# Kernel tuning notes

Hardware: AMD Instinct MI355X
Metric: run time of the kernel (lower is better)

Reference implementation:

```python
import jax, jax.numpy as jnp
import numpy as np

B, S, D = 8, 1024, 768
H, DK = 12, 64
DFF = 3072
EPS = 1e-5


def setup_inputs() -> dict:
    key = jax.random.key(0)
    ks = jax.random.split(key, 12)
    s = lambda fan_in: 1.0 / np.sqrt(fan_in)
    return {
        "x": jax.random.normal(ks[0], (B, S, D), jnp.float32),
        "Wq": jax.random.normal(ks[1], (D, D), jnp.float32) * s(D),
        "Wk": jax.random.normal(ks[2], (D, D), jnp.float32) * s(D),
        "Wv": jax.random.normal(ks[3], (D, D), jnp.float32) * s(D),
        "Wo": jax.random.normal(ks[4], (D, D), jnp.float32) * s(D),
        "g1": jnp.ones((D,), jnp.float32),
        "b1": jnp.zeros((D,), jnp.float32),
        "g2": jnp.ones((D,), jnp.float32),
        "b2": jnp.zeros((D,), jnp.float32),
        "W1": jax.random.normal(ks[5], (D, DFF), jnp.float32) * s(D),
        "bW1": jnp.zeros((DFF,), jnp.float32),
        "W2": jax.random.normal(ks[6], (DFF, D), jnp.float32) * s(DFF),
        "bW2": jnp.zeros((D,), jnp.float32),
    }


def _layernorm(x, g, b):
    mu = x.mean(-1, keepdims=True)
    var = ((x - mu) ** 2).mean(-1, keepdims=True)
    return (x - mu) * jax.lax.rsqrt(var + EPS) * g + b


def reference(x, Wq, Wk, Wv, Wo, g1, b1, g2, b2, W1, bW1, W2, bW2):
    scale = DK ** (-0.5)
    # pre-norm attention block
    h = _layernorm(x, g1, b1)
    q = (h @ Wq).reshape(B, S, H, DK)
    k = (h @ Wk).reshape(B, S, H, DK)
    v = (h @ Wv).reshape(B, S, H, DK)
    logits = jnp.einsum("bqhd,bkhd->bhqk", q, k) * scale  # [B,H,S,S]
    weights = jax.nn.softmax(logits, axis=-1)
    attn = jnp.einsum("bhqk,bkhd->bqhd", weights, v).reshape(B, S, D)
    x = x + attn @ Wo
    # pre-norm FFN block
    h = _layernorm(x, g2, b2)
    h = jax.nn.gelu(h @ W1 + bW1, approximate=False)
    x = x + h @ W2 + bW2
    return x
```

## Files before the change

kernel.cpp:

```cpp
#include <hip/hip_runtime.h>
#include <cstdint>
#include <cstddef>

#define B_   8
#define S_   1024
#define D_   768
#define H_   12
#define DK_  64
#define DFF_ 3072
#define M_   (B_*S_)

typedef __attribute__((ext_vector_type(8))) short  short8;
typedef __attribute__((ext_vector_type(4))) short  short4v;
typedef __attribute__((ext_vector_type(8))) __bf16 bf16x8;
typedef __attribute__((ext_vector_type(4))) float  f32x4;
typedef __attribute__((ext_vector_type(4))) unsigned uint4v;
typedef __attribute__((ext_vector_type(2))) unsigned uint2v;

__device__ __forceinline__ unsigned short f2bf(float f) {
    unsigned u = __builtin_bit_cast(unsigned, f);
    u += 0x7FFFu + ((u >> 16) & 1u);
    return (unsigned short)(u >> 16);
}

__device__ __forceinline__ unsigned pkbf(float a, float b) {
    unsigned short ua = __builtin_bit_cast(unsigned short, (__bf16)a);
    unsigned short ub = __builtin_bit_cast(unsigned short, (__bf16)b);
    return (unsigned)ua | ((unsigned)ub << 16);
}

__device__ __forceinline__ f32x4 mfma16(short8 a, short8 b, f32x4 c) {
    return __builtin_amdgcn_mfma_f32_16x16x32_bf16(
        __builtin_bit_cast(bf16x8, a), __builtin_bit_cast(bf16x8, b), c, 0, 0, 0);
}

__device__ __forceinline__ void gload16(const void* g, void* l) {
    auto gp = reinterpret_cast<const __attribute__((address_space(1))) unsigned*>(
        reinterpret_cast<uintptr_t>(g));
    auto lp = reinterpret_cast<__attribute__((address_space(3))) unsigned*>(
        reinterpret_cast<uintptr_t>(l));
    __builtin_amdgcn_global_load_lds(gp, lp, 16, 0, 0);
}

__device__ __forceinline__ float gelu_fast(float v) {
    float w = v * __builtin_fmaf(v * v, 0.044715f, 1.0f);
    float e = __builtin_amdgcn_exp2f(-2.3021178f * w);
    return v * __builtin_amdgcn_rcpf(1.0f + e);
}

__global__ __launch_bounds__(256) void wtrans12_kernel(
    const float* __restrict__ Wq, const float* __restrict__ Wk,
    const float* __restrict__ Wv, const float* __restrict__ Wo,
    const float* __restrict__ W1, const float* __restrict__ W2,
    unsigned short* __restrict__ wt_qkv, unsigned short* __restrict__ wt_1,
    unsigned short* __restrict__ wt_2)
{
    __shared__ float tile[32][33];
    const int z = blockIdx.z;
    const float* src; unsigned short* dst; int sstride, dstride;
    if (z < 4) {
        src = (z == 0) ? Wq : (z == 1) ? Wk : (z == 2) ? Wv : Wo;
        dst = wt_qkv + (size_t)z * 768 * 768;
        sstride = 768; dstride = 768;
    } else if (z < 8) {
        int q = z - 4;
        src = W1 + q * 768;
        dst = wt_1 + (size_t)q * 768 * 768;
        sstride = 3072; dstride = 768;
    } else {
        int q = z - 8;
        src = W2 + (size_t)q * 768 * 768;
        dst = wt_2 + q * 768;
        sstride = 768; dstride = 3072;
    }
    const int n0 = blockIdx.x * 32, k0 = blockIdx.y * 32;
    const int tx = threadIdx.x, ty = threadIdx.y;
#pragma unroll
    for (int j = 0; j < 4; ++j)
        tile[ty + j*8][tx] = src[(size_t)(k0 + ty + j*8) * sstride + n0 + tx];
    __syncthreads();
#pragma unroll
    for (int j = 0; j < 4; ++j)
        dst[(size_t)(n0 + ty + j*8) * dstride + k0 + tx] = f2bf(tile[tx][ty + j*8]);
}

__global__ __launch_bounds__(256) void ln_kernel(
    const float* __restrict__ x, const float* __restrict__ g,
    const float* __restrict__ b, unsigned short* __restrict__ out)
{
    int row = blockIdx.x, t = threadIdx.x;
    const float* xr = x + (size_t)row * D_;
    float v[3];
#pragma unroll
    for (int i = 0; i < 3; ++i) v[i] = xr[t + i*256];
    float s  = v[0] + v[1] + v[2];
    float ss = v[0]*v[0] + v[1]*v[1] + v[2]*v[2];
#pragma unroll
    for (int d = 1; d < 64; d <<= 1) { s += __shfl_xor(s, d); ss += __shfl_xor(ss, d); }
    __shared__ float red[8];
    int w = t >> 6, lane = t & 63;
    if (lane == 0) { red[w] = s; red[4 + w] = ss; }
    __syncthreads();
    s  = red[0] + red[1] + red[2] + red[3];
    ss = red[4] + red[5] + red[6] + red[7];
    float mu   = s * (1.0f / D_);
    float var  = ss * (1.0f / D_) - mu * mu;
    float rstd = rsqrtf(var + 1e-5f);
    unsigned short* orow = out + (size_t)row * D_;
#pragma unroll
    for (int i = 0; i < 3; ++i) {
        int c = t + i*256;
        orow[c] = f2bf((v[i] - mu) * rstd * g[c] + b[c]);
    }
}

template<int BN, int EPI>
__global__ __launch_bounds__(256, 2) void gemm_kernel(
    const unsigned short* __restrict__ A, const unsigned short* __restrict__ Wt,
    const float* __restrict__ bias, const float* __restrict__ resid,
    void* __restrict__ outp, int N, int K)
{
    __shared__ unsigned short Al[2][128*64];
    __shared__ unsigned short Bl[2][BN*64];
    constexpr int NJ = BN / 64;
    constexpr int ASH = 4, BSH = 2*NJ;
    const int nwg = gridDim.x;
    const int p = blockIdx.x;
    const int cpx = nwg >> 3;
    const int xcd = p & 7, id = p >> 3;
    const int nbn = N / BN;
    const int rowsX = cpx / nbn;
    const int hn = nbn >> 1, hc = cpx >> 1;
    const int half = id / hc, rr = id % hc;
    const int bm = xcd * rowsX + rr / hn;
    const int bn = half * hn + rr % hn;

    const int t = threadIdx.x;
    const int lane = t & 63, w = t >> 6;
    const int wm = w >> 1, wn = w & 1;
    const int lr = lane & 15, lh = lane >> 4;
    const char* aBase = (const char*)(A  + (size_t)(bm*128) * K);
    const char* bBase = (const char*)(Wt + (size_t)(bn*BN)  * K);

    uintptr_t aAdr[ASH], bAdr[BSH];
#pragma unroll
    for (int s = 0; s < ASH; ++s) {
        int d = s*4096 + t*16;
        int row = d >> 7;
        int ch  = ((d >> 4) & 7) ^ (row & 7);
        aAdr[s] = (uintptr_t)aBase + (size_t)row*(K*2) + ch*16;
    }
#pragma unroll
    for (int s = 0; s < BSH; ++s) {
        int d = s*4096 + t*16;
        int row = d >> 7;
        int ch  = ((d >> 4) & 7) ^ (row & 7);
        bAdr[s] = (uintptr_t)bBase + (size_t)row*(K*2) + ch*16;
    }

    f32x4 acc[4][2*NJ] = {};

    auto stage = [&](int kt, int buf) {
        const int k0b = kt << 7;
#pragma unroll
        for (int s = 0; s < ASH; ++s)
            gload16((const void*)(aAdr[s] + k0b), (char*)&Al[buf][0] + s*4096 + t*16);
#pragma unroll
        for (int s = 0; s < BSH; ++s)
            gload16((const void*)(bAdr[s] + k0b), (char*)&Bl[buf][0] + s*4096 + t*16);
    };

    const int nk = K >> 6;
    stage(0, 0);
    stage(1, 1);

    for (int it = 0; it < nk; ++it) {
        const int buf = it & 1;
        if (it + 1 < nk) {
            if constexpr (BN == 128) asm volatile("s_waitcnt vmcnt(8)" ::: "memory");
            else                     asm volatile("s_waitcnt vmcnt(6)" ::: "memory");
        } else {
            asm volatile("s_waitcnt vmcnt(0)" ::: "memory");
        }
        __builtin_amdgcn_s_barrier();

        short8 xf[2][4], wf[2][2*NJ];
#pragma unroll
        for (int kk = 0; kk < 2; ++kk) {
#pragma unroll
            for (int i = 0; i < 4; ++i)
                xf[kk][i] = *reinterpret_cast<const short8*>(
                    &Al[buf][(wm*64 + i*16 + lr)*64 + (((kk*4 + lh) ^ (lr & 7))*8)]);
#pragma unroll
            for (int j = 0; j < 2*NJ; ++j)
                wf[kk][j] = *reinterpret_cast<const short8*>(
                    &Bl[buf][(wn*(32*NJ) + j*16 + lr)*64 + (((kk*4 + lh) ^ (lr & 7))*8)]);
        }
        __builtin_amdgcn_s_setprio(1);
#pragma unroll
        for (int kk = 0; kk < 2; ++kk)
#pragma unroll
            for (int i = 0; i < 4; ++i)
#pragma unroll
                for (int j = 0; j < 2*NJ; ++j)
                    acc[i][j] = mfma16(wf[kk][j], xf[kk][i], acc[i][j]);
        __builtin_amdgcn_s_setprio(0);
        __builtin_amdgcn_s_barrier();
        if (it + 2 < nk) stage(it + 2, buf);
    }

#pragma unroll
    for (int i = 0; i < 4; ++i) {
        const int m = bm*128 + wm*64 + i*16 + lr;
#pragma unroll
        for (int j = 0; j < 2*NJ; ++j) {
            const int n0 = bn*BN + wn*(32*NJ) + j*16 + lh*4;
            f32x4 v = acc[i][j];
            if (EPI == 1) {
                f32x4 bb = *reinterpret_cast<const f32x4*>(&bias[n0]);
                v += bb;
#pragma unroll
                for (int r = 0; r < 4; ++r) v[r] = gelu_fast(v[r]);
            }
            if (EPI == 2) {
                if (bias) v += *reinterpret_cast<const f32x4*>(&bias[n0]);
                v += *reinterpret_cast<const f32x4*>(&resid[(size_t)m*N + n0]);
                *reinterpret_cast<f32x4*>(&((float*)outp)[(size_t)m*N + n0]) = v;
            } else {
                uint2v pv = { pkbf(v[0], v[1]), pkbf(v[2], v[3]) };
                *reinterpret_cast<uint2v*>(&((unsigned short*)outp)[(size_t)m*N + n0]) = pv;
            }
        }
    }
}

__global__ __launch_bounds__(256) void vtrans_kernel(
    const unsigned short* __restrict__ qkv, unsigned short* __restrict__ vt)
{
    __shared__ unsigned short tl[64][65];
    int bid = blockIdx.x;
    int sblk = bid & 15, bh = bid >> 4;
    int b = bh / H_, h = bh % H_;
    int t = threadIdx.x, tx = t & 63, ty = t >> 6;
    int s0 = sblk * 64;
#pragma unroll
    for (int j = 0; j < 16; ++j) {
        int s = j*4 + ty;
        tl[s][tx] = qkv[(size_t)(b*S_ + s0 + s)*2304 + 1536 + h*64 + tx];
    }
    __syncthreads();
#pragma unroll
    for (int j = 0; j < 16; ++j) {
        int dk = j*4 + ty;
        vt[((size_t)bh*64 + dk)*S_ + s0 + tx] = tl[tx][dk];
    }
}

__global__ __launch_bounds__(512) void attn_kernel(
    const unsigned short* __restrict__ qkv, const unsigned short* __restrict__ vt,
    unsigned short* __restrict__ out)
{
    __shared__ unsigned short Kl[2][64*64];
    __shared__ unsigned short Vl[2][64*64];

    const int p = blockIdx.x;
    const int l = (p & 7) * 48 + (p >> 3);
    const int qb = l & 3, bh = l >> 2;
    const int b = bh / H_, h = bh % H_;
    const int t = threadIdx.x, lane = t & 63, w = t >> 6;
    const int lr = lane & 15, lh = lane >> 4;
    const int sz = (lr & 7) << 3;

    const float SC = 0.125f * 1.44269504089f;
    const float SHIFT = 12.0f;

    const int qrow0 = qb*256 + w*32;
    short8 bq[2][2];
#pragma unroll
    for (int qi = 0; qi < 2; ++qi) {
        const unsigned short* qp = qkv + (size_t)(b*S_ + qrow0 + qi*16 + lr)*2304 + h*64;
#pragma unroll
        for (int c = 0; c < 2; ++c)
            bq[qi][c] = *reinterpret_cast<const short8*>(&qp[c*32 + lh*8]);
    }

    float l_run[2] = {0.f, 0.f};
    f32x4 o[2][4] = {};

    uintptr_t kAdr, vAdr;
    {
        int d = t*16;
        int row = d >> 7;
        int sc = (d & 127) ^ ((row & 7) << 4);
        kAdr = (uintptr_t)qkv + ((size_t)(b*S_ + row)*2304 + 768 + h*64)*2 + sc;
        vAdr = (uintptr_t)vt  + ((size_t)(bh*64 + row)*1024)*2 + sc;
    }

    auto stage = [&](int kb, int buf) {
        const size_t kOff = (size_t)kb * 64 * 2304 * 2;
        const size_t vOff = (size_t)kb * 128;
        gload16((const void*)(kAdr + kOff), (char*)&Kl[buf][0] + t*16);
        gload16((const void*)(vAdr + vOff), (char*)&Vl[buf][0] + t*16);
    };

    stage(0, 0);
    asm volatile("s_waitcnt vmcnt(0)" ::: "memory");
    __builtin_amdgcn_s_barrier();

    for (int kb = 0; kb < 16; ++kb) {
        const int buf = kb & 1;
        if (kb < 15) stage(kb + 1, buf ^ 1);

        short8 ak[4][2];
#pragma unroll
        for (int j = 0; j < 4; ++j)
#pragma unroll
            for (int c = 0; c < 2; ++c)
                ak[j][c] = *reinterpret_cast<const short8*>(
                    &Kl[buf][(j*16 + lr)*64 + ((c*32 + lh*8) ^ sz)]);

        short8 av[4][2];
#pragma unroll
        for (int j = 0; j < 4; ++j) {
            const unsigned short* vrow = &Vl[buf][(j*16 + lr)*64];
#pragma unroll
            for (int ks = 0; ks < 2; ++ks) {
                short4v lo = *reinterpret_cast<const short4v*>(&vrow[(ks*32 + lh*4)      ^ sz]);
                short4v hi = *reinterpret_cast<const short4v*>(&vrow[(ks*32 + 16 + lh*4) ^ sz]);
                av[j][ks] = __builtin_shufflevector(lo, hi, 0,1,2,3,4,5,6,7);
            }
        }

#pragma unroll
        for (int qi = 0; qi < 2; ++qi) {
            f32x4 s[4];
            __builtin_amdgcn_s_setprio(1);
#pragma unroll
            for (int j = 0; j < 4; ++j) {
                f32x4 z = {0.f, 0.f, 0.f, 0.f};
                z = mfma16(ak[j][0], bq[qi][0], z);
                z = mfma16(ak[j][1], bq[qi][1], z);
                s[j] = z;
            }
            __builtin_amdgcn_s_setprio(0);

            float rs = 0.f;
#pragma unroll
            for (int j = 0; j < 4; ++j)
#pragma unroll
                for (int r = 0; r < 4; ++r) {
                    float pv = __builtin_amdgcn_exp2f(
                        __builtin_fmaf(s[j][r], SC, -SHIFT));
                    s[j][r] = pv;
                    rs += pv;
                }
            l_run[qi] += rs;

            uint4v u0 = { pkbf(s[0][0], s[0][1]), pkbf(s[0][2], s[0][3]),
                          pkbf(s[1][0], s[1][1]), pkbf(s[1][2], s[1][3]) };
            uint4v u1 = { pkbf(s[2][0], s[2][1]), pkbf(s[2][2], s[2][3]),
                          pkbf(s[3][0], s[3][1]), pkbf(s[3][2], s[3][3]) };
            short8 pb0 = __builtin_bit_cast(short8, u0);
            short8 pb1 = __builtin_bit_cast(short8, u1);

            __builtin_amdgcn_s_setprio(1);
#pragma unroll
            for (int j = 0; j < 4; ++j) {
                o[qi][j] = mfma16(av[j][0], pb0, o[qi][j]);
                o[qi][j] = mfma16(av[j][1], pb1, o[qi][j]);
            }
            __builtin_amdgcn_s_setprio(0);
        }

        asm volatile("s_waitcnt vmcnt(0)" ::: "memory");
        __builtin_amdgcn_s_barrier();
    }

#pragma unroll
    for (int qi = 0; qi < 2; ++qi) {
        float ls = l_run[qi];
        ls += __shfl_xor(ls, 16);
        ls += __shfl_xor(ls, 32);
        float inv = 1.0f / ls;
        int q = qrow0 + qi*16 + lr;
        unsigned short* orow = out + (size_t)(b*S_ + q)*D_ + h*64;
#pragma unroll
        for (int j = 0; j < 4; ++j) {
            uint2v vv = { pkbf(o[qi][j][0]*inv, o[qi][j][1]*inv),
                          pkbf(o[qi][j][2]*inv, o[qi][j][3]*inv) };
            *reinterpret_cast<uint2v*>(&orow[j*16 + lh*4]) = vv;
        }
    }
}

extern "C" void kernel_launch(void* const* d_in, const int* in_sizes, int n_in,
                              void* d_out, int out_size, void* d_ws, size_t ws_size,
                              hipStream_t stream)
{
    (void)in_sizes; (void)n_in; (void)out_size; (void)ws_size;
    const float* x   = (const float*)d_in[0];
    const float* Wq  = (const float*)d_in[1];
    const float* Wk  = (const float*)d_in[2];
    const float* Wv  = (const float*)d_in[3];
    const float* Wo  = (const float*)d_in[4];
    const float* g1  = (const float*)d_in[5];
    const float* b1  = (const float*)d_in[6];
    const float* g2  = (const float*)d_in[7];
    const float* b2  = (const float*)d_in[8];
    const float* W1  = (const float*)d_in[9];
    const float* bW1 = (const float*)d_in[10];
    const float* W2  = (const float*)d_in[11];
    const float* bW2 = (const float*)d_in[12];
    float* out = (float*)d_out;

    char* ws = (char*)d_ws;
    unsigned short* wt_qkv = (unsigned short*)(ws);
    unsigned short* wt_o   = (unsigned short*)(ws + 3538944);
    unsigned short* wt_1   = (unsigned short*)(ws + 4718592);
    unsigned short* wt_2   = (unsigned short*)(ws + 9437184);
    unsigned short* slotA  = (unsigned short*)(ws + 14155776);
    unsigned short* qkv    = (unsigned short*)(ws + 26738688);
    unsigned short* vt     = (unsigned short*)(ws + 64487424);
    unsigned short* ffm    = qkv;

    dim3 tb(32, 8);
    wtrans12_kernel<<<dim3(24,24,12), tb, 0, stream>>>(
        Wq, Wk, Wv, Wo, W1, W2, wt_qkv, wt_1, wt_2);

    ln_kernel<<<M_, 256, 0, stream>>>(x, g1, b1, slotA);
    gemm_kernel<128,0><<<1152, 256, 0, stream>>>(slotA, wt_qkv, nullptr, nullptr, qkv, 2304, 768);
    vtrans_kernel<<<1536, 256, 0, stream>>>(qkv, vt);
    attn_kernel<<<384, 512, 0, stream>>>(qkv, vt, slotA);
    gemm_kernel<64,2><<<768, 256, 0, stream>>>(slotA, wt_o, nullptr, x, (void*)out, 768, 768);
    ln_kernel<<<M_, 256, 0, stream>>>(out, g2, b2, slotA);
    gemm_kernel<128,1><<<1536, 256, 0, stream>>>(slotA, wt_1, bW1, nullptr, ffm, 3072, 768);
    gemm_kernel<64,2><<<768, 256, 0, stream>>>(ffm, wt_2, bW2, out, (void*)out, 768, 3072);
}
```

Before: 272.3 us.

## Pre-permute V transpose for single 16B LDS reads; halve attention block size

The V-transpose kernel now writes each 64-key chunk in a permuted column order. This lets the attention kernel load each V fragment with one 16-byte LDS read instead of two 8-byte reads plus a shuffle. The attention launch also changes from 384 blocks of 512 threads covering 256 query rows to 768 blocks of 256 threads covering 128 rows, with each thread staging two K/V chunks. The launch bound requests 3 blocks per CU. Smaller blocks should help occupancy and load balance, at the cost of reloading K/V tiles twice as often per query row.

```diff
diff --git a/kernel.cpp b/kernel.cpp
--- a/kernel.cpp
+++ b/kernel.cpp
@@ -11,7 +11,6 @@
 #define M_   (B_*S_)
 
 typedef __attribute__((ext_vector_type(8))) short  short8;
-typedef __attribute__((ext_vector_type(4))) short  short4v;
 typedef __attribute__((ext_vector_type(8))) __bf16 bf16x8;
 typedef __attribute__((ext_vector_type(4))) float  f32x4;
 typedef __attribute__((ext_vector_type(4))) unsigned uint4v;
@@ -249,14 +248,17 @@
         tl[s][tx] = qkv[(size_t)(b*S_ + s0 + s)*2304 + 1536 + h*64 + tx];
     }
     __syncthreads();
+    const int lh2 = (tx >> 3) & 3, e2 = tx & 7;
+    const int psrc = (tx & 32) |
+        ((e2 < 4) ? (lh2*4 + e2) : (16 + lh2*4 + (e2 - 4)));
 #pragma unroll
     for (int j = 0; j < 16; ++j) {
         int dk = j*4 + ty;
-        vt[((size_t)bh*64 + dk)*S_ + s0 + tx] = tl[tx][dk];
-    }
-}
-
-__global__ __launch_bounds__(512) void attn_kernel(
+        vt[((size_t)bh*64 + dk)*S_ + s0 + tx] = tl[psrc][dk];
+    }
+}
+
+__global__ __launch_bounds__(256, 3) void attn_kernel(
     const unsigned short* __restrict__ qkv, const unsigned short* __restrict__ vt,
     unsigned short* __restrict__ out)
 {
@@ -264,8 +266,8 @@
     __shared__ unsigned short Vl[2][64*64];
 
     const int p = blockIdx.x;
-    const int l = (p & 7) * 48 + (p >> 3);
-    const int qb = l & 3, bh = l >> 2;
+    const int l = (p & 7) * 96 + (p >> 3);
+    const int qb = l & 7, bh = l >> 3;
     const int b = bh / H_, h = bh % H_;
     const int t = threadIdx.x, lane = t & 63, w = t >> 6;
     const int lr = lane & 15, lh = lane >> 4;
@@ -274,7 +276,7 @@
     const float SC = 0.125f * 1.44269504089f;
     const float SHIFT = 12.0f;
 
-    const int qrow0 = qb*256 + w*32;
+    const int qrow0 = qb*128 + w*32;
     short8 bq[2][2];
 #pragma unroll
     for (int qi = 0; qi < 2; ++qi) {
@@ -287,20 +289,25 @@
     float l_run[2] = {0.f, 0.f};
     f32x4 o[2][4] = {};
 
-    uintptr_t kAdr, vAdr;
-    {
-        int d = t*16;
+    uintptr_t kAdr[2], vAdr[2];
+#pragma unroll
+    for (int shot = 0; shot < 2; ++shot) {
+        int d = shot*4096 + t*16;
         int row = d >> 7;
         int sc = (d & 127) ^ ((row & 7) << 4);
-        kAdr = (uintptr_t)qkv + ((size_t)(b*S_ + row)*2304 + 768 + h*64)*2 + sc;
-        vAdr = (uintptr_t)vt  + ((size_t)(bh*64 + row)*1024)*2 + sc;
+        kAdr[shot] = (uintptr_t)qkv + ((size_t)(b*S_ + row)*2304 + 768 + h*64)*2 + sc;
+        vAdr[shot] = (uintptr_t)vt  + ((size_t)(bh*64 + row)*1024)*2 + sc;
     }
 
     auto stage = [&](int kb, int buf) {
         const size_t kOff = (size_t)kb * 64 * 2304 * 2;
         const size_t vOff = (size_t)kb * 128;
-        gload16((const void*)(kAdr + kOff), (char*)&Kl[buf][0] + t*16);
-        gload16((const void*)(vAdr + vOff), (char*)&Vl[buf][0] + t*16);
+#pragma unroll
+        for (int shot = 0; shot < 2; ++shot) {
+            int d = shot*4096 + t*16;
+            gload16((const void*)(kAdr[shot] + kOff), (char*)&Kl[buf][0] + d);
+            gload16((const void*)(vAdr[shot] + vOff), (char*)&Vl[buf][0] + d);
+        }
     };
 
     stage(0, 0);
@@ -324,11 +331,9 @@
         for (int j = 0; j < 4; ++j) {
             const unsigned short* vrow = &Vl[buf][(j*16 + lr)*64];
 #pragma unroll
-            for (int ks = 0; ks < 2; ++ks) {
-                short4v lo = *reinterpret_cast<const short4v*>(&vrow[(ks*32 + lh*4)      ^ sz]);
-                short4v hi = *reinterpret_cast<const short4v*>(&vrow[(ks*32 + 16 + lh*4) ^ sz]);
-                av[j][ks] = __builtin_shufflevector(lo, hi, 0,1,2,3,4,5,6,7);
-            }
+            for (int ks = 0; ks < 2; ++ks)
+                av[j][ks] = *reinterpret_cast<const short8*>(
+                    &vrow[(ks*32 + lh*8) ^ sz]);
         }
 
 #pragma unroll
@@ -430,7 +435,7 @@
     ln_kernel<<<M_, 256, 0, stream>>>(x, g1, b1, slotA);
     gemm_kernel<128,0><<<1152, 256, 0, stream>>>(slotA, wt_qkv, nullptr, nullptr, qkv, 2304, 768);
     vtrans_kernel<<<1536, 256, 0, stream>>>(qkv, vt);
-    attn_kernel<<<384, 512, 0, stream>>>(qkv, vt, slotA);
+    attn_kernel<<<768, 256, 0, stream>>>(qkv, vt, slotA);
     gemm_kernel<64,2><<<768, 256, 0, stream>>>(slotA, wt_o, nullptr, x, (void*)out, 768, 768);
     ln_kernel<<<M_, 256, 0, stream>>>(out, g2, b2, slotA);
     gemm_kernel<128,1><<<1536, 256, 0, stream>>>(slotA, wt_1, bW1, nullptr, ffm, 3072, 768);
```

Result: faster. 251.6 us, median of 2 (-7.6%).
